# Kernel tuning notes

Measured on AMD Instinct MI355X. Metric: run time of the kernel, lower is better.

Reference implementation:

```python
import jax, jax.numpy as jnp
import numpy as np

EXPLORATION_C = 10.0
NEG_FILL = float(np.log(1e-45))  # matches torch.log(tensor(1e-45))


def setup_inputs() -> dict:
    key = jax.random.key(0)
    ks = jax.random.split(key, 10)
    B, U, S, H = 16, 500, 256, 128
    return {
        "user_input_seq_with_stay": jax.random.normal(ks[0], (B, U, 4), jnp.float32),
        "server_input_seq": jax.random.uniform(ks[1], (B, S, 6), jnp.float32),
        "masks": jax.random.randint(ks[2], (B, U, S), 0, 2) > 0,
        "Wu": jax.random.normal(ks[3], (3, H), jnp.float32) * 0.1,
        "bu": jax.random.normal(ks[4], (H,), jnp.float32) * 0.1,
        "Ws": jax.random.normal(ks[5], (7, H), jnp.float32) * 0.1,
        "bs": jax.random.normal(ks[6], (H,), jnp.float32) * 0.1,
        "W1": jax.random.normal(ks[7], (H, H), jnp.float32) * 0.1,
        "W2": jax.random.normal(ks[8], (H, H), jnp.float32) * 0.1,
        "vt": jax.random.normal(ks[9], (H,), jnp.float32) * 0.1,
    }


def reference(user_input_seq_with_stay, server_input_seq, masks,
              Wu, bu, Ws, bs, W1, W2, vt):
    # Drop the stay column: user_input_seq = [..., :-1]  -> [B, U, 3]
    user_input = user_input_seq_with_stay[..., :-1]
    user_enc = user_input @ Wu + bu  # [B, U, H] (UserEncoder, all steps at once)

    B, S, _ = server_input_seq.shape
    # server_seq = cat(static[:, :, :2], tmp_capacity[:, :, 2:], active)
    # server_allocate_mat is never updated in the loop -> active column is all zero.
    active = jnp.zeros((B, S, 1), server_input_seq.dtype)
    server_seq = jnp.concatenate([server_input_seq, active], axis=-1)  # [B, S, 7]
    server_enc = server_seq @ Ws + bs  # [B, S, H] (identical every decode step)

    enc_t = server_enc @ W1            # [B, S, H]
    dec_t = user_enc @ W2              # [B, U, H]
    # Additive attention score for every (user step, server) pair.
    u_i = jnp.tanh(enc_t[:, None, :, :] + dec_t[:, :, None, :]) @ vt  # [B, U, S]
    score = jnp.where(masks, u_i, jnp.asarray(NEG_FILL, u_i.dtype)) * EXPLORATION_C
    probs = jax.nn.softmax(score, axis=-1)  # [B, U, S]
    return probs
```

## Files before the change

### kernel.cpp

```cpp
#include <hip/hip_runtime.h>

#define B_ 16
#define U_ 500
#define S_ 256
#define H_ 128
#define UTILE 32
#define NWAVES 16
#define TPB (NWAVES * 64)

__global__ __launch_bounds__(TPB, 1) void attn_kernel(
    const float* __restrict__ user,
    const float* __restrict__ server,
    const int*   __restrict__ masks,
    const float* __restrict__ Wu,
    const float* __restrict__ bu,
    const float* __restrict__ Ws,
    const float* __restrict__ bs,
    const float* __restrict__ W1,
    const float* __restrict__ W2,
    const float* __restrict__ vt,
    float* __restrict__ out)
{
  __shared__ float E[H_][S_];
  __shared__ float M1s[6 * H_];
  __shared__ float M2s[3 * H_];
  __shared__ float c1s[H_];
  __shared__ float c2s[H_];
  __shared__ float vts[H_];
  __shared__ float decs[NWAVES][2][H_];
  __shared__ float vsum_s;

  const int tid = threadIdx.x;
  const int bid = blockIdx.x;
  const int b   = bid >> 4;
  const int u0  = (bid & 15) * UTILE;

  {
    const int h = tid & (H_ - 1);
    for (int job = tid >> 7; job < 11; job += 8) {
      const float* Lv; const float* Rm; float* dst;
      if (job < 6)       { Lv = Ws + job * H_;       Rm = W1; dst = M1s + job * H_; }
      else if (job == 6) { Lv = bs;                  Rm = W1; dst = c1s; }
      else if (job < 10) { Lv = Wu + (job - 7) * H_; Rm = W2; dst = M2s + (job - 7) * H_; }
      else               { Lv = bu;                  Rm = W2; dst = c2s; }
      float acc = 0.f;
      for (int j = 0; j < H_; ++j) acc = fmaf(Lv[j], Rm[j * H_ + h], acc);
      dst[h] = acc;
    }
    if (tid < H_) vts[tid] = vt[tid];
    if (tid < 64) {
      float v = vt[tid] + vt[tid + 64];
      #pragma unroll
      for (int off = 32; off > 0; off >>= 1) v += __shfl_xor(v, off, 64);
      if (tid == 0) vsum_s = v;
    }
  }

  int lflag;
  {
    int4 mw = *reinterpret_cast<const int4*>(masks + tid * 4);
    lflag = ((unsigned)mw.x > 1u) | ((unsigned)mw.y > 1u) |
            ((unsigned)mw.z > 1u) | ((unsigned)mw.w > 1u);
  }
  const int bytemode = __syncthreads_or(lflag);

  {
    const int s  = tid & (S_ - 1);
    const int h0 = tid >> 8;
    const float2* sv = reinterpret_cast<const float2*>(server + ((size_t)b * S_ + s) * 6);
    const float2 p0 = sv[0], p1 = sv[1], p2 = sv[2];
    for (int h = h0; h < H_; h += 4) {
      float a = c1s[h];
      a = fmaf(p0.x, M1s[0 * H_ + h], a);
      a = fmaf(p0.y, M1s[1 * H_ + h], a);
      a = fmaf(p1.x, M1s[2 * H_ + h], a);
      a = fmaf(p1.y, M1s[3 * H_ + h], a);
      a = fmaf(p2.x, M1s[4 * H_ + h], a);
      a = fmaf(p2.y, M1s[5 * H_ + h], a);
      E[h][s] = __expf(fminf(fmaxf(a + a, -60.f), 60.f));
    }
  }

  const int w    = tid >> 6;
  const int lane = tid & 63;
  const int uA   = u0 + 2 * w;
  const int uAc  = min(uA,     U_ - 1);
  const int uBc  = min(uA + 1, U_ - 1);

  {
    const float* uvA = user + ((size_t)b * U_ + uAc) * 4;
    const float* uvB = user + ((size_t)b * U_ + uBc) * 4;
    const float gA0 = uvA[0], gA1 = uvA[1], gA2 = uvA[2];
    const float gB0 = uvB[0], gB1 = uvB[1], gB2 = uvB[2];
    #pragma unroll
    for (int r = 0; r < 2; ++r) {
      const int h1 = lane, h2 = lane + 64;
      const float g0 = r ? gB0 : gA0, g1 = r ? gB1 : gA1, g2 = r ? gB2 : gA2;
      float a0 = c2s[h1];
      a0 = fmaf(g0, M2s[0 * H_ + h1], a0);
      a0 = fmaf(g1, M2s[1 * H_ + h1], a0);
      a0 = fmaf(g2, M2s[2 * H_ + h1], a0);
      decs[w][r][h1] = __expf(fminf(fmaxf(a0 + a0, -60.f), 60.f));
      float a1 = c2s[h2];
      a1 = fmaf(g0, M2s[0 * H_ + h2], a1);
      a1 = fmaf(g1, M2s[1 * H_ + h2], a1);
      a1 = fmaf(g2, M2s[2 * H_ + h2], a1);
      decs[w][r][h2] = __expf(fminf(fmaxf(a1 + a1, -60.f), 60.f));
    }
  }
  __syncthreads();

  const size_t ridxA = ((size_t)b * U_ + uAc) * S_ + (size_t)lane * 4;
  const size_t ridxB = ((size_t)b * U_ + uBc) * S_ + (size_t)lane * 4;
  int mA0, mA1, mA2, mA3, mB0, mB1, mB2, mB3;
  if (!bytemode) {
    int4 mm = *reinterpret_cast<const int4*>(masks + ridxA);
    mA0 = mm.x; mA1 = mm.y; mA2 = mm.z; mA3 = mm.w;
    int4 nn = *reinterpret_cast<const int4*>(masks + ridxB);
    mB0 = nn.x; mB1 = nn.y; mB2 = nn.z; mB3 = nn.w;
  } else {
    const unsigned char* mb = reinterpret_cast<const unsigned char*>(masks);
    uchar4 mm = *reinterpret_cast<const uchar4*>(mb + ridxA);
    mA0 = mm.x; mA1 = mm.y; mA2 = mm.z; mA3 = mm.w;
    uchar4 nn = *reinterpret_cast<const uchar4*>(mb + ridxB);
    mB0 = nn.x; mB1 = nn.y; mB2 = nn.z; mB3 = nn.w;
  }

  float aA0 = 0.f, aA1 = 0.f, aA2 = 0.f, aA3 = 0.f;
  float aB0 = 0.f, aB1 = 0.f, aB2 = 0.f, aB3 = 0.f;
  #pragma unroll 4
  for (int h4 = 0; h4 < H_ / 4; ++h4) {
    const float4 e0 = *reinterpret_cast<const float4*>(&E[h4 * 4 + 0][lane * 4]);
    const float4 e1 = *reinterpret_cast<const float4*>(&E[h4 * 4 + 1][lane * 4]);
    const float4 e2 = *reinterpret_cast<const float4*>(&E[h4 * 4 + 2][lane * 4]);
    const float4 e3 = *reinterpret_cast<const float4*>(&E[h4 * 4 + 3][lane * 4]);
    const float4 dA = *reinterpret_cast<const float4*>(&decs[w][0][h4 * 4]);
    const float4 dB = *reinterpret_cast<const float4*>(&decs[w][1][h4 * 4]);
    const float4 v4 = *reinterpret_cast<const float4*>(&vts[h4 * 4]);

    auto quad = [&v4](float ea, float eb, float ec, float ed, const float4& d, float& acc) {
      float t0 = fmaf(ea, d.x, 1.0f);
      float t1 = fmaf(eb, d.y, 1.0f);
      float t2 = fmaf(ec, d.z, 1.0f);
      float t3 = fmaf(ed, d.w, 1.0f);
      float t01 = t0 * t1;
      float t23 = t2 * t3;
      float n01 = fmaf(v4.x, t1, v4.y * t0);
      float n23 = fmaf(v4.z, t3, v4.w * t2);
      float den = t01 * t23;
      float num = fmaf(n01, t23, n23 * t01);
      acc = fmaf(num, __builtin_amdgcn_rcpf(den), acc);
    };
    quad(e0.x, e1.x, e2.x, e3.x, dA, aA0);
    quad(e0.y, e1.y, e2.y, e3.y, dA, aA1);
    quad(e0.z, e1.z, e2.z, e3.z, dA, aA2);
    quad(e0.w, e1.w, e2.w, e3.w, dA, aA3);
    quad(e0.x, e1.x, e2.x, e3.x, dB, aB0);
    quad(e0.y, e1.y, e2.y, e3.y, dB, aB1);
    quad(e0.z, e1.z, e2.z, e3.z, dB, aB2);
    quad(e0.w, e1.w, e2.w, e3.w, dB, aB3);
  }

  if (uA < U_) {
    const float negs = -103.6163291847321f * 10.0f;
    const float vs10 = vsum_s * 10.0f;
    #pragma unroll
    for (int r = 0; r < 2; ++r) {
      const float b0 = r ? aB0 : aA0, b1 = r ? aB1 : aA1;
      const float b2 = r ? aB2 : aA2, b3 = r ? aB3 : aA3;
      const int   m0 = r ? mB0 : mA0, m1 = r ? mB1 : mA1;
      const int   m2 = r ? mB2 : mA2, m3 = r ? mB3 : mA3;
      float s0 = m0 ? fmaf(-20.0f, b0, vs10) : negs;
      float s1 = m1 ? fmaf(-20.0f, b1, vs10) : negs;
      float s2 = m2 ? fmaf(-20.0f, b2, vs10) : negs;
      float s3 = m3 ? fmaf(-20.0f, b3, vs10) : negs;
      float mx = fmaxf(fmaxf(s0, s1), fmaxf(s2, s3));
      #pragma unroll
      for (int off = 32; off > 0; off >>= 1) mx = fmaxf(mx, __shfl_xor(mx, off, 64));
      float p0 = __expf(s0 - mx);
      float p1 = __expf(s1 - mx);
      float p2 = __expf(s2 - mx);
      float p3 = __expf(s3 - mx);
      float sum = (p0 + p1) + (p2 + p3);
      #pragma unroll
      for (int off = 32; off > 0; off >>= 1) sum += __shfl_xor(sum, off, 64);
      const float inv = __builtin_amdgcn_rcpf(sum);
      float4 o;
      o.x = p0 * inv; o.y = p1 * inv; o.z = p2 * inv; o.w = p3 * inv;
      *reinterpret_cast<float4*>(out + (r ? ridxB : ridxA)) = o;
    }
  }
}

extern "C" void kernel_launch(void* const* d_in, const int* in_sizes, int n_in,
                              void* d_out, int out_size, void* d_ws, size_t ws_size,
                              hipStream_t stream) {
  const float* user   = (const float*)d_in[0];
  const float* server = (const float*)d_in[1];
  const int*   masks  = (const int*)d_in[2];
  const float* Wu = (const float*)d_in[3];
  const float* bu = (const float*)d_in[4];
  const float* Ws = (const float*)d_in[5];
  const float* bs = (const float*)d_in[6];
  const float* W1 = (const float*)d_in[7];
  const float* W2 = (const float*)d_in[8];
  const float* vt = (const float*)d_in[9];
  float* out = (float*)d_out;
  (void)in_sizes; (void)n_in; (void)out_size; (void)d_ws; (void)ws_size;

  attn_kernel<<<dim3(B_ * ((U_ + UTILE - 1) / UTILE)), dim3(TPB), 0, stream>>>(
      user, server, masks, Wu, bu, Ws, bs, W1, W2, vt, out);
}
```

Baseline: 44.49 us.

## Retile attention so wave pairs share four user rows across split server halves

Each pair of waves now handles four user rows, with each wave covering half of the 256 servers at two servers per lane, in place of one wave doing two rows across all servers. Each E element loaded from LDS is reused across four decoder rows, so fewer E bytes are read per FLOP. The cost is two extra block-wide barriers and shared-memory reductions for the softmax max and sum across the two halves. vt is now read straight from global memory instead of a shared copy, and stores shrink to float2.

```diff
diff --git a/kernel.cpp b/kernel.cpp
--- a/kernel.cpp
+++ b/kernel.cpp
@@ -26,8 +26,9 @@
   __shared__ float M2s[3 * H_];
   __shared__ float c1s[H_];
   __shared__ float c2s[H_];
-  __shared__ float vts[H_];
-  __shared__ float decs[NWAVES][2][H_];
+  __shared__ float decs[8][4][H_];
+  __shared__ float redmax[8][4][2];
+  __shared__ float redsum[8][4][2];
   __shared__ float vsum_s;
 
   const int tid = threadIdx.x;
@@ -47,7 +48,6 @@
       for (int j = 0; j < H_; ++j) acc = fmaf(Lv[j], Rm[j * H_ + h], acc);
       dst[h] = acc;
     }
-    if (tid < H_) vts[tid] = vt[tid];
     if (tid < 64) {
       float v = vt[tid] + vt[tid + 64];
       #pragma unroll
@@ -83,111 +83,123 @@
 
   const int w    = tid >> 6;
   const int lane = tid & 63;
-  const int uA   = u0 + 2 * w;
-  const int uAc  = min(uA,     U_ - 1);
-  const int uBc  = min(uA + 1, U_ - 1);
-
-  {
-    const float* uvA = user + ((size_t)b * U_ + uAc) * 4;
-    const float* uvB = user + ((size_t)b * U_ + uBc) * 4;
-    const float gA0 = uvA[0], gA1 = uvA[1], gA2 = uvA[2];
-    const float gB0 = uvB[0], gB1 = uvB[1], gB2 = uvB[2];
-    #pragma unroll
-    for (int r = 0; r < 2; ++r) {
-      const int h1 = lane, h2 = lane + 64;
-      const float g0 = r ? gB0 : gA0, g1 = r ? gB1 : gA1, g2 = r ? gB2 : gA2;
-      float a0 = c2s[h1];
-      a0 = fmaf(g0, M2s[0 * H_ + h1], a0);
-      a0 = fmaf(g1, M2s[1 * H_ + h1], a0);
-      a0 = fmaf(g2, M2s[2 * H_ + h1], a0);
-      decs[w][r][h1] = __expf(fminf(fmaxf(a0 + a0, -60.f), 60.f));
-      float a1 = c2s[h2];
-      a1 = fmaf(g0, M2s[0 * H_ + h2], a1);
-      a1 = fmaf(g1, M2s[1 * H_ + h2], a1);
-      a1 = fmaf(g2, M2s[2 * H_ + h2], a1);
-      decs[w][r][h2] = __expf(fminf(fmaxf(a1 + a1, -60.f), 60.f));
+  const int rg   = w >> 1;
+  const int sh   = w & 1;
+  const int s0   = sh * 128 + 2 * lane;
+
+  {
+    #pragma unroll
+    for (int rr = 0; rr < 2; ++rr) {
+      const int r  = 2 * sh + rr;
+      const int uc = min(u0 + rg * 4 + r, U_ - 1);
+      const float* uv = user + ((size_t)b * U_ + uc) * 4;
+      const float g0 = uv[0], g1 = uv[1], g2 = uv[2];
+      #pragma unroll
+      for (int hh = 0; hh < 2; ++hh) {
+        const int h = lane + hh * 64;
+        float a = c2s[h];
+        a = fmaf(g0, M2s[0 * H_ + h], a);
+        a = fmaf(g1, M2s[1 * H_ + h], a);
+        a = fmaf(g2, M2s[2 * H_ + h], a);
+        decs[rg][r][h] = __expf(fminf(fmaxf(a + a, -60.f), 60.f));
+      }
     }
   }
   __syncthreads();
 
-  const size_t ridxA = ((size_t)b * U_ + uAc) * S_ + (size_t)lane * 4;
-  const size_t ridxB = ((size_t)b * U_ + uBc) * S_ + (size_t)lane * 4;
-  int mA0, mA1, mA2, mA3, mB0, mB1, mB2, mB3;
+  size_t ridx[4]; int uval[4]; int m0[4], m1[4];
+  #pragma unroll
+  for (int r = 0; r < 4; ++r) {
+    const int u = u0 + rg * 4 + r;
+    uval[r] = (u < U_);
+    ridx[r] = ((size_t)b * U_ + min(u, U_ - 1)) * S_ + s0;
+  }
   if (!bytemode) {
-    int4 mm = *reinterpret_cast<const int4*>(masks + ridxA);
-    mA0 = mm.x; mA1 = mm.y; mA2 = mm.z; mA3 = mm.w;
-    int4 nn = *reinterpret_cast<const int4*>(masks + ridxB);
-    mB0 = nn.x; mB1 = nn.y; mB2 = nn.z; mB3 = nn.w;
+    #pragma unroll
+    for (int r = 0; r < 4; ++r) {
+      int2 mm = *reinterpret_cast<const int2*>(masks + ridx[r]);
+      m0[r] = mm.x; m1[r] = mm.y;
+    }
   } else {
     const unsigned char* mb = reinterpret_cast<const unsigned char*>(masks);
-    uchar4 mm = *reinterpret_cast<const uchar4*>(mb + ridxA);
-    mA0 = mm.x; mA1 = mm.y; mA2 = mm.z; mA3 = mm.w;
-    uchar4 nn = *reinterpret_cast<const uchar4*>(mb + ridxB);
-    mB0 = nn.x; mB1 = nn.y; mB2 = nn.z; mB3 = nn.w;
-  }
-
-  float aA0 = 0.f, aA1 = 0.f, aA2 = 0.f, aA3 = 0.f;
-  float aB0 = 0.f, aB1 = 0.f, aB2 = 0.f, aB3 = 0.f;
+    #pragma unroll
+    for (int r = 0; r < 4; ++r) {
+      uchar2 mm = *reinterpret_cast<const uchar2*>(mb + ridx[r]);
+      m0[r] = mm.x; m1[r] = mm.y;
+    }
+  }
+
+  float acc[4][2] = {{0.f,0.f},{0.f,0.f},{0.f,0.f},{0.f,0.f}};
+
+  auto quad = [](const float4& vv, float ea, float eb, float ec, float ed,
+                 const float4& d, float& a) {
+    float t0 = fmaf(ea, d.x, 1.0f);
+    float t1 = fmaf(eb, d.y, 1.0f);
+    float t2 = fmaf(ec, d.z, 1.0f);
+    float t3 = fmaf(ed, d.w, 1.0f);
+    float t01 = t0 * t1;
+    float t23 = t2 * t3;
+    float n01 = fmaf(vv.x, t1, vv.y * t0);
+    float n23 = fmaf(vv.z, t3, vv.w * t2);
+    float den = t01 * t23;
+    float num = fmaf(n01, t23, n23 * t01);
+    a = fmaf(num, __builtin_amdgcn_rcpf(den), a);
+  };
+
   #pragma unroll 4
   for (int h4 = 0; h4 < H_ / 4; ++h4) {
-    const float4 e0 = *reinterpret_cast<const float4*>(&E[h4 * 4 + 0][lane * 4]);
-    const float4 e1 = *reinterpret_cast<const float4*>(&E[h4 * 4 + 1][lane * 4]);
-    const float4 e2 = *reinterpret_cast<const float4*>(&E[h4 * 4 + 2][lane * 4]);
-    const float4 e3 = *reinterpret_cast<const float4*>(&E[h4 * 4 + 3][lane * 4]);
-    const float4 dA = *reinterpret_cast<const float4*>(&decs[w][0][h4 * 4]);
-    const float4 dB = *reinterpret_cast<const float4*>(&decs[w][1][h4 * 4]);
-    const float4 v4 = *reinterpret_cast<const float4*>(&vts[h4 * 4]);
-
-    auto quad = [&v4](float ea, float eb, float ec, float ed, const float4& d, float& acc) {
-      float t0 = fmaf(ea, d.x, 1.0f);
-      float t1 = fmaf(eb, d.y, 1.0f);
-      float t2 = fmaf(ec, d.z, 1.0f);
-      float t3 = fmaf(ed, d.w, 1.0f);
-      float t01 = t0 * t1;
-      float t23 = t2 * t3;
-      float n01 = fmaf(v4.x, t1, v4.y * t0);
-      float n23 = fmaf(v4.z, t3, v4.w * t2);
-      float den = t01 * t23;
-      float num = fmaf(n01, t23, n23 * t01);
-      acc = fmaf(num, __builtin_amdgcn_rcpf(den), acc);
-    };
-    quad(e0.x, e1.x, e2.x, e3.x, dA, aA0);
-    quad(e0.y, e1.y, e2.y, e3.y, dA, aA1);
-    quad(e0.z, e1.z, e2.z, e3.z, dA, aA2);
-    quad(e0.w, e1.w, e2.w, e3.w, dA, aA3);
-    quad(e0.x, e1.x, e2.x, e3.x, dB, aB0);
-    quad(e0.y, e1.y, e2.y, e3.y, dB, aB1);
-    quad(e0.z, e1.z, e2.z, e3.z, dB, aB2);
-    quad(e0.w, e1.w, e2.w, e3.w, dB, aB3);
-  }
-
-  if (uA < U_) {
-    const float negs = -103.6163291847321f * 10.0f;
-    const float vs10 = vsum_s * 10.0f;
-    #pragma unroll
-    for (int r = 0; r < 2; ++r) {
-      const float b0 = r ? aB0 : aA0, b1 = r ? aB1 : aA1;
-      const float b2 = r ? aB2 : aA2, b3 = r ? aB3 : aA3;
-      const int   m0 = r ? mB0 : mA0, m1 = r ? mB1 : mA1;
-      const int   m2 = r ? mB2 : mA2, m3 = r ? mB3 : mA3;
-      float s0 = m0 ? fmaf(-20.0f, b0, vs10) : negs;
-      float s1 = m1 ? fmaf(-20.0f, b1, vs10) : negs;
-      float s2 = m2 ? fmaf(-20.0f, b2, vs10) : negs;
-      float s3 = m3 ? fmaf(-20.0f, b3, vs10) : negs;
-      float mx = fmaxf(fmaxf(s0, s1), fmaxf(s2, s3));
-      #pragma unroll
-      for (int off = 32; off > 0; off >>= 1) mx = fmaxf(mx, __shfl_xor(mx, off, 64));
-      float p0 = __expf(s0 - mx);
-      float p1 = __expf(s1 - mx);
-      float p2 = __expf(s2 - mx);
-      float p3 = __expf(s3 - mx);
-      float sum = (p0 + p1) + (p2 + p3);
-      #pragma unroll
-      for (int off = 32; off > 0; off >>= 1) sum += __shfl_xor(sum, off, 64);
-      const float inv = __builtin_amdgcn_rcpf(sum);
-      float4 o;
-      o.x = p0 * inv; o.y = p1 * inv; o.z = p2 * inv; o.w = p3 * inv;
-      *reinterpret_cast<float4*>(out + (r ? ridxB : ridxA)) = o;
+    const int hh = h4 * 4;
+    const float2 e0 = *reinterpret_cast<const float2*>(&E[hh + 0][s0]);
+    const float2 e1 = *reinterpret_cast<const float2*>(&E[hh + 1][s0]);
+    const float2 e2 = *reinterpret_cast<const float2*>(&E[hh + 2][s0]);
+    const float2 e3 = *reinterpret_cast<const float2*>(&E[hh + 3][s0]);
+    const float4 d0 = *reinterpret_cast<const float4*>(&decs[rg][0][hh]);
+    const float4 d1 = *reinterpret_cast<const float4*>(&decs[rg][1][hh]);
+    const float4 d2 = *reinterpret_cast<const float4*>(&decs[rg][2][hh]);
+    const float4 d3 = *reinterpret_cast<const float4*>(&decs[rg][3][hh]);
+    const float4 vv = *reinterpret_cast<const float4*>(vt + hh);
+    quad(vv, e0.x, e1.x, e2.x, e3.x, d0, acc[0][0]);
+    quad(vv, e0.y, e1.y, e2.y, e3.y, d0, acc[0][1]);
+    quad(vv, e0.x, e1.x, e2.x, e3.x, d1, acc[1][0]);
+    quad(vv, e0.y, e1.y, e2.y, e3.y, d1, acc[1][1]);
+    quad(vv, e0.x, e1.x, e2.x, e3.x, d2, acc[2][0]);
+    quad(vv, e0.y, e1.y, e2.y, e3.y, d2, acc[2][1]);
+    quad(vv, e0.x, e1.x, e2.x, e3.x, d3, acc[3][0]);
+    quad(vv, e0.y, e1.y, e2.y, e3.y, d3, acc[3][1]);
+  }
+
+  const float negs = -103.6163291847321f * 10.0f;
+  const float vs10 = vsum_s * 10.0f;
+  float p[4][2];
+  #pragma unroll
+  for (int r = 0; r < 4; ++r) {
+    float sA = m0[r] ? fmaf(-20.0f, acc[r][0], vs10) : negs;
+    float sB = m1[r] ? fmaf(-20.0f, acc[r][1], vs10) : negs;
+    p[r][0] = sA; p[r][1] = sB;
+    float mx = fmaxf(sA, sB);
+    #pragma unroll
+    for (int off = 32; off > 0; off >>= 1) mx = fmaxf(mx, __shfl_xor(mx, off, 64));
+    if (lane == 0) redmax[rg][r][sh] = mx;
+  }
+  __syncthreads();
+  #pragma unroll
+  for (int r = 0; r < 4; ++r) {
+    const float gmx = fmaxf(redmax[rg][r][0], redmax[rg][r][1]);
+    float pa = __expf(p[r][0] - gmx);
+    float pb = __expf(p[r][1] - gmx);
+    p[r][0] = pa; p[r][1] = pb;
+    float sm = pa + pb;
+    #pragma unroll
+    for (int off = 32; off > 0; off >>= 1) sm += __shfl_xor(sm, off, 64);
+    if (lane == 0) redsum[rg][r][sh] = sm;
+  }
+  __syncthreads();
+  #pragma unroll
+  for (int r = 0; r < 4; ++r) {
+    if (uval[r]) {
+      const float inv = __builtin_amdgcn_rcpf(redsum[rg][r][0] + redsum[rg][r][1]);
+      float2 o; o.x = p[r][0] * inv; o.y = p[r][1] * inv;
+      *reinterpret_cast<float2*>(out + ridx[r]) = o;
     }
   }
 }
```

After: 49.03 us. 10.2% more time.

## Split hidden dimension into two halves to shrink LDS footprint

Applied to the files above, without the earlier changes.

The precomputed server tanh-exponential table E and per-wave decoder buffers now cover only half of the hidden dimension at a time, and the kernel makes two passes with a barrier between them. This roughly halves shared memory per block, and launch bounds change from 1 to 8 so more blocks can be resident per CU. The factor of two in the pre-activation is folded into the precomputed M1/M2/c constants. In exchange it adds an extra barrier and recomputes E per pass, with less overlap inside each block.

```diff
diff --git a/kernel.cpp b/kernel.cpp
--- a/kernel.cpp
+++ b/kernel.cpp
@@ -7,8 +7,9 @@
 #define UTILE 32
 #define NWAVES 16
 #define TPB (NWAVES * 64)
-
-__global__ __launch_bounds__(TPB, 1) void attn_kernel(
+#define HHALF 64
+
+__global__ __launch_bounds__(TPB, 8) void attn_kernel(
     const float* __restrict__ user,
     const float* __restrict__ server,
     const int*   __restrict__ masks,
@@ -21,13 +22,13 @@
     const float* __restrict__ vt,
     float* __restrict__ out)
 {
-  __shared__ float E[H_][S_];
+  __shared__ float E[HHALF][S_];
   __shared__ float M1s[6 * H_];
   __shared__ float M2s[3 * H_];
   __shared__ float c1s[H_];
   __shared__ float c2s[H_];
   __shared__ float vts[H_];
-  __shared__ float decs[NWAVES][2][H_];
+  __shared__ float decs[NWAVES][2][HHALF];
   __shared__ float vsum_s;
 
   const int tid = threadIdx.x;
@@ -45,7 +46,7 @@
       else               { Lv = bu;                  Rm = W2; dst = c2s; }
       float acc = 0.f;
       for (int j = 0; j < H_; ++j) acc = fmaf(Lv[j], Rm[j * H_ + h], acc);
-      dst[h] = acc;
+      dst[h] = acc + acc;
     }
     if (tid < H_) vts[tid] = vt[tid];
     if (tid < 64) {
@@ -64,51 +65,21 @@
   }
   const int bytemode = __syncthreads_or(lflag);
 
-  {
-    const int s  = tid & (S_ - 1);
-    const int h0 = tid >> 8;
-    const float2* sv = reinterpret_cast<const float2*>(server + ((size_t)b * S_ + s) * 6);
-    const float2 p0 = sv[0], p1 = sv[1], p2 = sv[2];
-    for (int h = h0; h < H_; h += 4) {
-      float a = c1s[h];
-      a = fmaf(p0.x, M1s[0 * H_ + h], a);
-      a = fmaf(p0.y, M1s[1 * H_ + h], a);
-      a = fmaf(p1.x, M1s[2 * H_ + h], a);
-      a = fmaf(p1.y, M1s[3 * H_ + h], a);
-      a = fmaf(p2.x, M1s[4 * H_ + h], a);
-      a = fmaf(p2.y, M1s[5 * H_ + h], a);
-      E[h][s] = __expf(fminf(fmaxf(a + a, -60.f), 60.f));
-    }
-  }
-
   const int w    = tid >> 6;
   const int lane = tid & 63;
   const int uA   = u0 + 2 * w;
   const int uAc  = min(uA,     U_ - 1);
   const int uBc  = min(uA + 1, U_ - 1);
 
-  {
-    const float* uvA = user + ((size_t)b * U_ + uAc) * 4;
-    const float* uvB = user + ((size_t)b * U_ + uBc) * 4;
-    const float gA0 = uvA[0], gA1 = uvA[1], gA2 = uvA[2];
-    const float gB0 = uvB[0], gB1 = uvB[1], gB2 = uvB[2];
-    #pragma unroll
-    for (int r = 0; r < 2; ++r) {
-      const int h1 = lane, h2 = lane + 64;
-      const float g0 = r ? gB0 : gA0, g1 = r ? gB1 : gA1, g2 = r ? gB2 : gA2;
-      float a0 = c2s[h1];
-      a0 = fmaf(g0, M2s[0 * H_ + h1], a0);
-      a0 = fmaf(g1, M2s[1 * H_ + h1], a0);
-      a0 = fmaf(g2, M2s[2 * H_ + h1], a0);
-      decs[w][r][h1] = __expf(fminf(fmaxf(a0 + a0, -60.f), 60.f));
-      float a1 = c2s[h2];
-      a1 = fmaf(g0, M2s[0 * H_ + h2], a1);
-      a1 = fmaf(g1, M2s[1 * H_ + h2], a1);
-      a1 = fmaf(g2, M2s[2 * H_ + h2], a1);
-      decs[w][r][h2] = __expf(fminf(fmaxf(a1 + a1, -60.f), 60.f));
-    }
-  }
-  __syncthreads();
+  const float* uvA = user + ((size_t)b * U_ + uAc) * 4;
+  const float* uvB = user + ((size_t)b * U_ + uBc) * 4;
+  const float gA0 = uvA[0], gA1 = uvA[1], gA2 = uvA[2];
+  const float gB0 = uvB[0], gB1 = uvB[1], gB2 = uvB[2];
+
+  const int sStage = tid & (S_ - 1);
+  const int h0     = tid >> 8;
+  const float2* sv = reinterpret_cast<const float2*>(server + ((size_t)b * S_ + sStage) * 6);
+  const float2 p0 = sv[0], p1 = sv[1], p2 = sv[2];
 
   const size_t ridxA = ((size_t)b * U_ + uAc) * S_ + (size_t)lane * 4;
   const size_t ridxB = ((size_t)b * U_ + uBc) * S_ + (size_t)lane * 4;
@@ -128,37 +99,70 @@
 
   float aA0 = 0.f, aA1 = 0.f, aA2 = 0.f, aA3 = 0.f;
   float aB0 = 0.f, aB1 = 0.f, aB2 = 0.f, aB3 = 0.f;
-  #pragma unroll 4
-  for (int h4 = 0; h4 < H_ / 4; ++h4) {
-    const float4 e0 = *reinterpret_cast<const float4*>(&E[h4 * 4 + 0][lane * 4]);
-    const float4 e1 = *reinterpret_cast<const float4*>(&E[h4 * 4 + 1][lane * 4]);
-    const float4 e2 = *reinterpret_cast<const float4*>(&E[h4 * 4 + 2][lane * 4]);
-    const float4 e3 = *reinterpret_cast<const float4*>(&E[h4 * 4 + 3][lane * 4]);
-    const float4 dA = *reinterpret_cast<const float4*>(&decs[w][0][h4 * 4]);
-    const float4 dB = *reinterpret_cast<const float4*>(&decs[w][1][h4 * 4]);
-    const float4 v4 = *reinterpret_cast<const float4*>(&vts[h4 * 4]);
-
-    auto quad = [&v4](float ea, float eb, float ec, float ed, const float4& d, float& acc) {
-      float t0 = fmaf(ea, d.x, 1.0f);
-      float t1 = fmaf(eb, d.y, 1.0f);
-      float t2 = fmaf(ec, d.z, 1.0f);
-      float t3 = fmaf(ed, d.w, 1.0f);
-      float t01 = t0 * t1;
-      float t23 = t2 * t3;
-      float n01 = fmaf(v4.x, t1, v4.y * t0);
-      float n23 = fmaf(v4.z, t3, v4.w * t2);
-      float den = t01 * t23;
-      float num = fmaf(n01, t23, n23 * t01);
-      acc = fmaf(num, __builtin_amdgcn_rcpf(den), acc);
-    };
-    quad(e0.x, e1.x, e2.x, e3.x, dA, aA0);
-    quad(e0.y, e1.y, e2.y, e3.y, dA, aA1);
-    quad(e0.z, e1.z, e2.z, e3.z, dA, aA2);
-    quad(e0.w, e1.w, e2.w, e3.w, dA, aA3);
-    quad(e0.x, e1.x, e2.x, e3.x, dB, aB0);
-    quad(e0.y, e1.y, e2.y, e3.y, dB, aB1);
-    quad(e0.z, e1.z, e2.z, e3.z, dB, aB2);
-    quad(e0.w, e1.w, e2.w, e3.w, dB, aB3);
+
+  #pragma unroll 1
+  for (int pass = 0; pass < 2; ++pass) {
+    const int hbase = pass * HHALF;
+    if (pass) __syncthreads();
+
+    for (int hr = h0; hr < HHALF; hr += 4) {
+      const int h = hbase + hr;
+      float a = c1s[h];
+      a = fmaf(p0.x, M1s[0 * H_ + h], a);
+      a = fmaf(p0.y, M1s[1 * H_ + h], a);
+      a = fmaf(p1.x, M1s[2 * H_ + h], a);
+      a = fmaf(p1.y, M1s[3 * H_ + h], a);
+      a = fmaf(p2.x, M1s[4 * H_ + h], a);
+      a = fmaf(p2.y, M1s[5 * H_ + h], a);
+      E[hr][sStage] = __expf(fminf(fmaxf(a, -60.f), 60.f));
+    }
+    {
+      const int h = hbase + lane;
+      float a0 = c2s[h];
+      a0 = fmaf(gA0, M2s[0 * H_ + h], a0);
+      a0 = fmaf(gA1, M2s[1 * H_ + h], a0);
+      a0 = fmaf(gA2, M2s[2 * H_ + h], a0);
+      decs[w][0][lane] = __expf(fminf(fmaxf(a0, -60.f), 60.f));
+      float a1 = c2s[h];
+      a1 = fmaf(gB0, M2s[0 * H_ + h], a1);
+      a1 = fmaf(gB1, M2s[1 * H_ + h], a1);
+      a1 = fmaf(gB2, M2s[2 * H_ + h], a1);
+      decs[w][1][lane] = __expf(fminf(fmaxf(a1, -60.f), 60.f));
+    }
+    __syncthreads();
+
+    #pragma unroll 4
+    for (int h4 = 0; h4 < HHALF / 4; ++h4) {
+      const float4 e0 = *reinterpret_cast<const float4*>(&E[h4 * 4 + 0][lane * 4]);
+      const float4 e1 = *reinterpret_cast<const float4*>(&E[h4 * 4 + 1][lane * 4]);
+      const float4 e2 = *reinterpret_cast<const float4*>(&E[h4 * 4 + 2][lane * 4]);
+      const float4 e3 = *reinterpret_cast<const float4*>(&E[h4 * 4 + 3][lane * 4]);
+      const float4 dA = *reinterpret_cast<const float4*>(&decs[w][0][h4 * 4]);
+      const float4 dB = *reinterpret_cast<const float4*>(&decs[w][1][h4 * 4]);
+      const float4 v4 = *reinterpret_cast<const float4*>(&vts[hbase + h4 * 4]);
+
+      auto quad = [&v4](float ea, float eb, float ec, float ed, const float4& d, float& acc) {
+        float t0 = fmaf(ea, d.x, 1.0f);
+        float t1 = fmaf(eb, d.y, 1.0f);
+        float t2 = fmaf(ec, d.z, 1.0f);
+        float t3 = fmaf(ed, d.w, 1.0f);
+        float t01 = t0 * t1;
+        float t23 = t2 * t3;
+        float n01 = fmaf(v4.x, t1, v4.y * t0);
+        float n23 = fmaf(v4.z, t3, v4.w * t2);
+        float den = t01 * t23;
+        float num = fmaf(n01, t23, n23 * t01);
+        acc = fmaf(num, __builtin_amdgcn_rcpf(den), acc);
+      };
+      quad(e0.x, e1.x, e2.x, e3.x, dA, aA0);
+      quad(e0.y, e1.y, e2.y, e3.y, dA, aA1);
+      quad(e0.z, e1.z, e2.z, e3.z, dA, aA2);
+      quad(e0.w, e1.w, e2.w, e3.w, dA, aA3);
+      quad(e0.x, e1.x, e2.x, e3.x, dB, aB0);
+      quad(e0.y, e1.y, e2.y, e3.y, dB, aB1);
+      quad(e0.z, e1.z, e2.z, e3.z, dB, aB2);
+      quad(e0.w, e1.w, e2.w, e3.w, dB, aB3);
+    }
   }
 
   if (uA < U_) {
@@ -177,16 +181,16 @@
       float mx = fmaxf(fmaxf(s0, s1), fmaxf(s2, s3));
       #pragma unroll
       for (int off = 32; off > 0; off >>= 1) mx = fmaxf(mx, __shfl_xor(mx, off, 64));
-      float p0 = __expf(s0 - mx);
-      float p1 = __expf(s1 - mx);
-      float p2 = __expf(s2 - mx);
-      float p3 = __expf(s3 - mx);
-      float sum = (p0 + p1) + (p2 + p3);
+      float p0_ = __expf(s0 - mx);
+      float p1_ = __expf(s1 - mx);
+      float p2_ = __expf(s2 - mx);
+      float p3_ = __expf(s3 - mx);
+      float sum = (p0_ + p1_) + (p2_ + p3_);
       #pragma unroll
       for (int off = 32; off > 0; off >>= 1) sum += __shfl_xor(sum, off, 64);
       const float inv = __builtin_amdgcn_rcpf(sum);
       float4 o;
-      o.x = p0 * inv; o.y = p1 * inv; o.z = p2 * inv; o.w = p3 * inv;
+      o.x = p0_ * inv; o.y = p1_ * inv; o.z = p2_ * inv; o.w = p3_ * inv;
       *reinterpret_cast<float4*>(out + (r ? ridxB : ridxA)) = o;
     }
   }
```

New measurement: 49.81 us. 12.0% more time.

## Split hidden dimension across two blocks with partial sums and a separate softmax pass

Applied to the files above, without the earlier changes.

The fused kernel is split into two kernels. The first launches twice as many blocks, each handling half of the hidden dimension with half the shared memory, and writes partial scores to the output and to a workspace, with masked entries marked by a sentinel. The second kernel adds the two partials and applies the masked softmax. This raises block count and occupancy (grid 256 to 512), at the cost of an extra global round trip of a B*U*S float buffer, an extra launch, and recomputing the small weight projections in every block. It falls back to the original monolithic kernel when the workspace is too small.

```diff
diff --git a/kernel.cpp b/kernel.cpp
--- a/kernel.cpp
+++ b/kernel.cpp
@@ -7,19 +7,208 @@
 #define UTILE 32
 #define NWAVES 16
 #define TPB (NWAVES * 64)
-
-__global__ __launch_bounds__(TPB, 1) void attn_kernel(
-    const float* __restrict__ user,
-    const float* __restrict__ server,
-    const int*   __restrict__ masks,
-    const float* __restrict__ Wu,
-    const float* __restrict__ bu,
-    const float* __restrict__ Ws,
-    const float* __restrict__ bs,
-    const float* __restrict__ W1,
-    const float* __restrict__ W2,
+#define HHALF 64
+#define SENT 1e30f
+
+__global__ __launch_bounds__(TPB, 8) void attn_partial(
+    const float* __restrict__ user, const float* __restrict__ server,
+    const int* __restrict__ masks,
+    const float* __restrict__ Wu, const float* __restrict__ bu,
+    const float* __restrict__ Ws, const float* __restrict__ bs,
+    const float* __restrict__ W1, const float* __restrict__ W2,
     const float* __restrict__ vt,
-    float* __restrict__ out)
+    float* __restrict__ out, float* __restrict__ ws)
+{
+  __shared__ float E[HHALF][S_];
+  __shared__ float M1h[6 * HHALF];
+  __shared__ float M2h[3 * HHALF];
+  __shared__ float c1h[HHALF];
+  __shared__ float c2h[HHALF];
+  __shared__ float decs[NWAVES][2][HHALF];
+
+  const int tid   = threadIdx.x;
+  const int bid   = blockIdx.x;
+  const int pr    = bid >> 1;
+  const int hh    = bid & 1;
+  const int hbase = hh * HHALF;
+  const int b     = pr >> 4;
+  const int u0    = (pr & 15) * UTILE;
+
+  int4 mw = *reinterpret_cast<const int4*>(masks + tid * 4);
+
+  {
+    const int hl = tid & (HHALF - 1);
+    const int g  = tid >> 6;
+    if (g < 11) {
+      const float* Lv; const float* Rm; float* dst;
+      if (g < 6)       { Lv = Ws + g * H_;       Rm = W1; dst = M1h + g * HHALF; }
+      else if (g == 6) { Lv = bs;                Rm = W1; dst = c1h; }
+      else if (g < 10) { Lv = Wu + (g - 7) * H_; Rm = W2; dst = M2h + (g - 7) * HHALF; }
+      else             { Lv = bu;                Rm = W2; dst = c2h; }
+      const int h = hbase + hl;
+      float acc = 0.f;
+      for (int j = 0; j < H_; ++j) acc = fmaf(Lv[j], Rm[j * H_ + h], acc);
+      dst[hl] = acc + acc;
+    }
+  }
+  const int lflag = ((unsigned)mw.x > 1u) | ((unsigned)mw.y > 1u) |
+                    ((unsigned)mw.z > 1u) | ((unsigned)mw.w > 1u);
+  const int bytemode = __syncthreads_or(lflag);
+
+  {
+    const int s  = tid & (S_ - 1);
+    const int h0 = tid >> 8;
+    const float2* sv = reinterpret_cast<const float2*>(server + ((size_t)b * S_ + s) * 6);
+    const float2 p0 = sv[0], p1 = sv[1], p2 = sv[2];
+    for (int hr = h0; hr < HHALF; hr += 4) {
+      float a = c1h[hr];
+      a = fmaf(p0.x, M1h[0 * HHALF + hr], a);
+      a = fmaf(p0.y, M1h[1 * HHALF + hr], a);
+      a = fmaf(p1.x, M1h[2 * HHALF + hr], a);
+      a = fmaf(p1.y, M1h[3 * HHALF + hr], a);
+      a = fmaf(p2.x, M1h[4 * HHALF + hr], a);
+      a = fmaf(p2.y, M1h[5 * HHALF + hr], a);
+      E[hr][s] = __expf(fminf(fmaxf(a, -60.f), 60.f));
+    }
+  }
+
+  const int w    = tid >> 6;
+  const int lane = tid & 63;
+  const int uA   = u0 + 2 * w;
+  const int uAc  = min(uA,     U_ - 1);
+  const int uBc  = min(uA + 1, U_ - 1);
+
+  {
+    const float* uvA = user + ((size_t)b * U_ + uAc) * 4;
+    const float* uvB = user + ((size_t)b * U_ + uBc) * 4;
+    const float gA0 = uvA[0], gA1 = uvA[1], gA2 = uvA[2];
+    const float gB0 = uvB[0], gB1 = uvB[1], gB2 = uvB[2];
+    float a0 = c2h[lane];
+    a0 = fmaf(gA0, M2h[0 * HHALF + lane], a0);
+    a0 = fmaf(gA1, M2h[1 * HHALF + lane], a0);
+    a0 = fmaf(gA2, M2h[2 * HHALF + lane], a0);
+    decs[w][0][lane] = __expf(fminf(fmaxf(a0, -60.f), 60.f));
+    float a1 = c2h[lane];
+    a1 = fmaf(gB0, M2h[0 * HHALF + lane], a1);
+    a1 = fmaf(gB1, M2h[1 * HHALF + lane], a1);
+    a1 = fmaf(gB2, M2h[2 * HHALF + lane], a1);
+    decs[w][1][lane] = __expf(fminf(fmaxf(a1, -60.f), 60.f));
+  }
+  __syncthreads();
+
+  float aA0 = 0.f, aA1 = 0.f, aA2 = 0.f, aA3 = 0.f;
+  float aB0 = 0.f, aB1 = 0.f, aB2 = 0.f, aB3 = 0.f;
+  #pragma unroll 4
+  for (int h4 = 0; h4 < HHALF / 4; ++h4) {
+    const float4 e0 = *reinterpret_cast<const float4*>(&E[h4 * 4 + 0][lane * 4]);
+    const float4 e1 = *reinterpret_cast<const float4*>(&E[h4 * 4 + 1][lane * 4]);
+    const float4 e2 = *reinterpret_cast<const float4*>(&E[h4 * 4 + 2][lane * 4]);
+    const float4 e3 = *reinterpret_cast<const float4*>(&E[h4 * 4 + 3][lane * 4]);
+    const float4 dA = *reinterpret_cast<const float4*>(&decs[w][0][h4 * 4]);
+    const float4 dB = *reinterpret_cast<const float4*>(&decs[w][1][h4 * 4]);
+    const float4 v4 = *reinterpret_cast<const float4*>(vt + hbase + h4 * 4);
+
+    auto quad = [&v4](float ea, float eb, float ec, float ed, const float4& d, float& acc) {
+      float t0 = fmaf(ea, d.x, 1.0f);
+      float t1 = fmaf(eb, d.y, 1.0f);
+      float t2 = fmaf(ec, d.z, 1.0f);
+      float t3 = fmaf(ed, d.w, 1.0f);
+      float t01 = t0 * t1;
+      float t23 = t2 * t3;
+      float n01 = fmaf(v4.x, t1, v4.y * t0);
+      float n23 = fmaf(v4.z, t3, v4.w * t2);
+      acc = fmaf(fmaf(n01, t23, n23 * t01), __builtin_amdgcn_rcpf(t01 * t23), acc);
+    };
+    quad(e0.x, e1.x, e2.x, e3.x, dA, aA0);
+    quad(e0.y, e1.y, e2.y, e3.y, dA, aA1);
+    quad(e0.z, e1.z, e2.z, e3.z, dA, aA2);
+    quad(e0.w, e1.w, e2.w, e3.w, dA, aA3);
+    quad(e0.x, e1.x, e2.x, e3.x, dB, aB0);
+    quad(e0.y, e1.y, e2.y, e3.y, dB, aB1);
+    quad(e0.z, e1.z, e2.z, e3.z, dB, aB2);
+    quad(e0.w, e1.w, e2.w, e3.w, dB, aB3);
+  }
+
+  if (uA >= U_) return;
+  const size_t ridxA = ((size_t)b * U_ + uAc) * S_ + (size_t)lane * 4;
+  const size_t ridxB = ((size_t)b * U_ + uBc) * S_ + (size_t)lane * 4;
+
+  if (!hh) {
+    float4 o;
+    o.x = aA0; o.y = aA1; o.z = aA2; o.w = aA3;
+    *reinterpret_cast<float4*>(out + ridxA) = o;
+    o.x = aB0; o.y = aB1; o.z = aB2; o.w = aB3;
+    *reinterpret_cast<float4*>(out + ridxB) = o;
+  } else {
+    int mA0, mA1, mA2, mA3, mB0, mB1, mB2, mB3;
+    if (!bytemode) {
+      int4 mm = *reinterpret_cast<const int4*>(masks + ridxA);
+      mA0 = mm.x; mA1 = mm.y; mA2 = mm.z; mA3 = mm.w;
+      int4 nn = *reinterpret_cast<const int4*>(masks + ridxB);
+      mB0 = nn.x; mB1 = nn.y; mB2 = nn.z; mB3 = nn.w;
+    } else {
+      const unsigned char* mb = reinterpret_cast<const unsigned char*>(masks);
+      uchar4 mm = *reinterpret_cast<const uchar4*>(mb + ridxA);
+      mA0 = mm.x; mA1 = mm.y; mA2 = mm.z; mA3 = mm.w;
+      uchar4 nn = *reinterpret_cast<const uchar4*>(mb + ridxB);
+      mB0 = nn.x; mB1 = nn.y; mB2 = nn.z; mB3 = nn.w;
+    }
+    float4 o;
+    o.x = mA0 ? aA0 : SENT; o.y = mA1 ? aA1 : SENT;
+    o.z = mA2 ? aA2 : SENT; o.w = mA3 ? aA3 : SENT;
+    *reinterpret_cast<float4*>(ws + ridxA) = o;
+    o.x = mB0 ? aB0 : SENT; o.y = mB1 ? aB1 : SENT;
+    o.z = mB2 ? aB2 : SENT; o.w = mB3 ? aB3 : SENT;
+    *reinterpret_cast<float4*>(ws + ridxB) = o;
+  }
+}
+
+__global__ __launch_bounds__(TPB) void attn_finish(
+    const float* __restrict__ vt, float* __restrict__ out, const float* __restrict__ ws)
+{
+  const int tid  = threadIdx.x;
+  const int bid  = blockIdx.x;
+  const int w    = tid >> 6;
+  const int lane = tid & 63;
+  const int b    = bid >> 5;
+  const int u    = (bid & 31) * 16 + w;
+  if (u >= U_) return;
+
+  float v = vt[lane] + vt[lane + 64];
+  #pragma unroll
+  for (int off = 32; off > 0; off >>= 1) v += __shfl_xor(v, off, 64);
+  const float vs10 = v * 10.0f;
+
+  const size_t row = ((size_t)b * U_ + u) * S_ + (size_t)lane * 4;
+  const float4 P0 = *reinterpret_cast<const float4*>(out + row);
+  const float4 P1 = *reinterpret_cast<const float4*>(ws + row);
+  float s0 = fmaf(-20.0f, P0.x + P1.x, vs10);
+  float s1 = fmaf(-20.0f, P0.y + P1.y, vs10);
+  float s2 = fmaf(-20.0f, P0.z + P1.z, vs10);
+  float s3 = fmaf(-20.0f, P0.w + P1.w, vs10);
+  float mx = fmaxf(fmaxf(s0, s1), fmaxf(s2, s3));
+  #pragma unroll
+  for (int off = 32; off > 0; off >>= 1) mx = fmaxf(mx, __shfl_xor(mx, off, 64));
+  float p0 = __expf(s0 - mx);
+  float p1 = __expf(s1 - mx);
+  float p2 = __expf(s2 - mx);
+  float p3 = __expf(s3 - mx);
+  float sum = (p0 + p1) + (p2 + p3);
+  #pragma unroll
+  for (int off = 32; off > 0; off >>= 1) sum += __shfl_xor(sum, off, 64);
+  const float inv = __builtin_amdgcn_rcpf(sum);
+  float4 o;
+  o.x = p0 * inv; o.y = p1 * inv; o.z = p2 * inv; o.w = p3 * inv;
+  *reinterpret_cast<float4*>(out + row) = o;
+}
+
+__global__ __launch_bounds__(TPB, 1) void attn_mono(
+    const float* __restrict__ user, const float* __restrict__ server,
+    const int* __restrict__ masks,
+    const float* __restrict__ Wu, const float* __restrict__ bu,
+    const float* __restrict__ Ws, const float* __restrict__ bs,
+    const float* __restrict__ W1, const float* __restrict__ W2,
+    const float* __restrict__ vt, float* __restrict__ out)
 {
   __shared__ float E[H_][S_];
   __shared__ float M1s[6 * H_];
@@ -55,7 +244,6 @@
       if (tid == 0) vsum_s = v;
     }
   }
-
   int lflag;
   {
     int4 mw = *reinterpret_cast<const int4*>(masks + tid * 4);
@@ -63,7 +251,6 @@
             ((unsigned)mw.z > 1u) | ((unsigned)mw.w > 1u);
   }
   const int bytemode = __syncthreads_or(lflag);
-
   {
     const int s  = tid & (S_ - 1);
     const int h0 = tid >> 8;
@@ -80,13 +267,11 @@
       E[h][s] = __expf(fminf(fmaxf(a + a, -60.f), 60.f));
     }
   }
-
   const int w    = tid >> 6;
   const int lane = tid & 63;
   const int uA   = u0 + 2 * w;
   const int uAc  = min(uA,     U_ - 1);
   const int uBc  = min(uA + 1, U_ - 1);
-
   {
     const float* uvA = user + ((size_t)b * U_ + uAc) * 4;
     const float* uvB = user + ((size_t)b * U_ + uBc) * 4;
@@ -109,7 +294,6 @@
     }
   }
   __syncthreads();
-
   const size_t ridxA = ((size_t)b * U_ + uAc) * S_ + (size_t)lane * 4;
   const size_t ridxB = ((size_t)b * U_ + uBc) * S_ + (size_t)lane * 4;
   int mA0, mA1, mA2, mA3, mB0, mB1, mB2, mB3;
@@ -125,7 +309,6 @@
     uchar4 nn = *reinterpret_cast<const uchar4*>(mb + ridxB);
     mB0 = nn.x; mB1 = nn.y; mB2 = nn.z; mB3 = nn.w;
   }
-
   float aA0 = 0.f, aA1 = 0.f, aA2 = 0.f, aA3 = 0.f;
   float aB0 = 0.f, aB1 = 0.f, aB2 = 0.f, aB3 = 0.f;
   #pragma unroll 4
@@ -137,7 +320,6 @@
     const float4 dA = *reinterpret_cast<const float4*>(&decs[w][0][h4 * 4]);
     const float4 dB = *reinterpret_cast<const float4*>(&decs[w][1][h4 * 4]);
     const float4 v4 = *reinterpret_cast<const float4*>(&vts[h4 * 4]);
-
     auto quad = [&v4](float ea, float eb, float ec, float ed, const float4& d, float& acc) {
       float t0 = fmaf(ea, d.x, 1.0f);
       float t1 = fmaf(eb, d.y, 1.0f);
@@ -147,9 +329,7 @@
       float t23 = t2 * t3;
       float n01 = fmaf(v4.x, t1, v4.y * t0);
       float n23 = fmaf(v4.z, t3, v4.w * t2);
-      float den = t01 * t23;
-      float num = fmaf(n01, t23, n23 * t01);
-      acc = fmaf(num, __builtin_amdgcn_rcpf(den), acc);
+      acc = fmaf(fmaf(n01, t23, n23 * t01), __builtin_amdgcn_rcpf(t01 * t23), acc);
     };
     quad(e0.x, e1.x, e2.x, e3.x, dA, aA0);
     quad(e0.y, e1.y, e2.y, e3.y, dA, aA1);
@@ -160,7 +340,6 @@
     quad(e0.z, e1.z, e2.z, e3.z, dB, aB2);
     quad(e0.w, e1.w, e2.w, e3.w, dB, aB3);
   }
-
   if (uA < U_) {
     const float negs = -103.6163291847321f * 10.0f;
     const float vs10 = vsum_s * 10.0f;
@@ -206,8 +385,16 @@
   const float* W2 = (const float*)d_in[8];
   const float* vt = (const float*)d_in[9];
   float* out = (float*)d_out;
-  (void)in_sizes; (void)n_in; (void)out_size; (void)d_ws; (void)ws_size;
-
-  attn_kernel<<<dim3(B_ * ((U_ + UTILE - 1) / UTILE)), dim3(TPB), 0, stream>>>(
-      user, server, masks, Wu, bu, Ws, bs, W1, W2, vt, out);
+  (void)in_sizes; (void)n_in; (void)out_size;
+
+  const size_t need = (size_t)B_ * U_ * S_ * sizeof(float);
+  if (ws_size >= need) {
+    float* wsp = (float*)d_ws;
+    attn_partial<<<dim3(2 * B_ * 16), dim3(TPB), 0, stream>>>(
+        user, server, masks, Wu, bu, Ws, bs, W1, W2, vt, out, wsp);
+    attn_finish<<<dim3(B_ * 32), dim3(TPB), 0, stream>>>(vt, out, wsp);
+  } else {
+    attn_mono<<<dim3(B_ * 16), dim3(TPB), 0, stream>>>(
+        user, server, masks, Wu, bu, Ws, bs, W1, W2, vt, out);
+  }
 }
```

After: 45.60 us. 1.03x slower.
